# Performance work log

Hardware: AMD Instinct MI355X
Metric: run time of the kernel (lower is better)

The kernel has to match this reference:

```python
import math
import jax, jax.numpy as jnp
import numpy as np

N_NODES = 10000
N_EDGES = 160000
F_IN = 256
HID = 500
N_OUT = 100


def setup_inputs() -> dict:
    key = jax.random.key(0)
    ks = jax.random.split(key, 20)
    inp = {}
    inp['x'] = jax.random.normal(ks[0], (N_NODES, F_IN), jnp.float32)
    inp['edge_src'] = jax.random.randint(ks[1], (N_EDGES,), 0, N_NODES, jnp.int32)
    inp['edge_dst'] = jax.random.randint(ks[2], (N_EDGES,), 0, N_NODES, jnp.int32)
    inp['edge_weight'] = jax.random.uniform(ks[3], (N_EDGES,), jnp.float32)
    s1 = 1.0 / math.sqrt(F_IN)
    s2 = 1.0 / math.sqrt(HID)
    inp['W1_rel'] = jax.random.uniform(ks[4], (HID, F_IN), jnp.float32, -s1, s1)
    inp['b1'] = jax.random.uniform(ks[5], (HID,), jnp.float32, -s1, s1)
    inp['W1_root'] = jax.random.uniform(ks[6], (HID, F_IN), jnp.float32, -s1, s1)
    inp['p1_w'] = jax.random.uniform(ks[7], (HID,), jnp.float32, -s2, s2)
    inp['W2_rel'] = jax.random.uniform(ks[8], (HID, HID), jnp.float32, -s2, s2)
    inp['b2'] = jax.random.uniform(ks[9], (HID,), jnp.float32, -s2, s2)
    inp['W2_root'] = jax.random.uniform(ks[10], (HID, HID), jnp.float32, -s2, s2)
    inp['p2_w'] = jax.random.uniform(ks[11], (HID,), jnp.float32, -s2, s2)
    s3 = 1.0 / math.sqrt(1000)
    inp['lin1_W'] = jax.random.uniform(ks[12], (2000, 1000), jnp.float32, -s3, s3)
    inp['lin1_b'] = jax.random.uniform(ks[13], (2000,), jnp.float32, -s3, s3)
    s4 = 1.0 / math.sqrt(2000)
    inp['lin2_W'] = jax.random.uniform(ks[14], (4000, 2000), jnp.float32, -s4, s4)
    inp['lin2_b'] = jax.random.uniform(ks[15], (4000,), jnp.float32, -s4, s4)
    s5 = 1.0 / math.sqrt(4000)
    inp['lin3_W'] = jax.random.uniform(ks[16], (N_OUT, 4000), jnp.float32, -s5, s5)
    inp['lin3_b'] = jax.random.uniform(ks[17], (N_OUT,), jnp.float32, -s5, s5)
    return inp


def graph_conv(x, src, dst, w, W_rel, b_rel, W_root):
    # PyG GraphConv: out_i = W_rel @ sum_{j->i} w_ji * x_j + b + W_root @ x_i
    msg = x[src] * w[:, None]                              # [E, F]
    agg = jax.ops.segment_sum(msg, dst, num_segments=x.shape[0])
    return agg @ W_rel.T + b_rel + x @ W_root.T


def topk_pool(x, src, dst, w, p_w, ratio=0.5):
    # PyG TopKPooling: score = tanh(x @ p / ||p||); keep top-k; scale x by score.
    N = x.shape[0]
    k = int(math.ceil(ratio * N))
    score = jnp.tanh((x @ p_w) / jnp.linalg.norm(p_w))
    vals, perm = jax.lax.top_k(score, k)
    x_new = x[perm] * vals[:, None]
    # keep fixed-size edge list; dropped edges get weight 0 and point to node 0
    new_idx = jnp.zeros((N,), jnp.int32).at[perm].set(jnp.arange(k, dtype=jnp.int32))
    mask = jnp.zeros((N,), bool).at[perm].set(True)
    keep = mask[src] & mask[dst]
    src_new = jnp.where(keep, new_idx[src], 0)
    dst_new = jnp.where(keep, new_idx[dst], 0)
    w_new = jnp.where(keep, w, 0.0)
    return x_new, src_new, dst_new, w_new


def readout(x):
    # global max pool + global mean pool over the single graph -> [1, 2F]
    return jnp.concatenate([jnp.max(x, 0, keepdims=True), jnp.mean(x, 0, keepdims=True)], axis=1)


def reference(x, edge_src, edge_dst, edge_weight,
              W1_rel, b1, W1_root, p1_w,
              W2_rel, b2, W2_root, p2_w,
              lin1_W, lin1_b, lin2_W, lin2_b, lin3_W, lin3_b):
    h = jax.nn.relu(graph_conv(x, edge_src, edge_dst, edge_weight, W1_rel, b1, W1_root))
    h, s1, d1, w1 = topk_pool(h, edge_src, edge_dst, edge_weight, p1_w)
    x1 = readout(h)
    h = jax.nn.relu(graph_conv(h, s1, d1, w1, W2_rel, b2, W2_root))
    h, _, _, _ = topk_pool(h, s1, d1, w1, p2_w)
    x2 = readout(h)
    z = x1 + x2                                            # [1, 1000]
    z = jax.nn.relu(z @ lin1_W.T + lin1_b)
    z = jax.nn.relu(z @ lin2_W.T + lin2_b)                 # dropout is identity at eval
    return jax.nn.sigmoid(z @ lin3_W.T + lin3_b)
```

## Files before the change

kernel.cpp:

```cpp
#include <hip/hip_runtime.h>
#include <hip/hip_bf16.h>
#include <math.h>

#define NN1   10000
#define NE    160000
#define FIN   256
#define HID   500
#define K1    5000
#define NN2   5000
#define K2    2500

#define CSR_OFFS   0u
#define CSR_POS    10008u
#define CSR_SRC    20008u
#define CSR_W      180008u
#define OFF_AGG    340016u
#define OFF_H      2900016u
#define OFF_XP2    (OFF_H + 2500000u)
#define OFF_XP1    7900016u
#define OFF_SC1    10400016u
#define OFF_RK1    10410016u
#define OFF_SC2    10420016u
#define OFF_RK2    10425016u
#define OFF_RO     10430016u
#define OFF_Z      10432016u
#define OFF_T1     10433016u
#define OFF_T2     10435016u
#define OFF_INV    10439016u
#define OFF_CNT    10439024u
#define OFF_PM     10639024u
#define OFF_PS     10671024u
#define OFF_XB     10703024u
#define OFF_W1RB   11983024u
#define OFF_W1TB   12047024u
#define OFF_W2RB   12111024u
#define OFF_W2TB   12236024u
#define OFF_XP1B   12361024u
#define WS_FLOATS  13611024u

#define RCHUNK 500
#define ROSLAB1 64
#define ROSLAB2 32
#define RORPB   79

__device__ inline unsigned f2ord(float f) {
    unsigned u = __float_as_uint(f);
    return (u & 0x80000000u) ? ~u : (u | 0x80000000u);
}
__device__ inline unsigned long long rkey(float s, int j) {
    return ((unsigned long long)f2ord(s) << 32) | (unsigned)(0xFFFFFFFFu - (unsigned)j);
}
__device__ inline unsigned short bf16rn(float f) {
    unsigned u = __float_as_uint(f);
    u += 0x7FFFu + ((u >> 16) & 1u);
    return (unsigned short)(u >> 16);
}
__device__ inline float bf2f(unsigned short u) {
    return __uint_as_float((unsigned)u << 16);
}

typedef __attribute__((ext_vector_type(8))) short short8;
typedef __attribute__((ext_vector_type(4))) short short4v;
typedef __attribute__((ext_vector_type(4))) float floatx4;


__global__ __launch_bounds__(256) void k_prep(
    const float* __restrict__ x, unsigned short* __restrict__ xb,
    const float* __restrict__ w1r, unsigned short* __restrict__ w1rb,
    const float* __restrict__ w1t, unsigned short* __restrict__ w1tb,
    const float* __restrict__ w2r, unsigned short* __restrict__ w2rb,
    const float* __restrict__ w2t, unsigned short* __restrict__ w2tb,
    const float* __restrict__ p1, const float* __restrict__ p2,
    float* __restrict__ invn,
    const int* __restrict__ edst, int* __restrict__ pos) {
    __shared__ float red[256];
    int y = blockIdx.y;
    if (y < 5) {
        const float* s; unsigned short* d; int n;
        switch (y) {
            case 0: s = x;   d = xb;   n = NN1 * FIN; break;
            case 1: s = w1r; d = w1rb; n = HID * FIN; break;
            case 2: s = w1t; d = w1tb; n = HID * FIN; break;
            case 3: s = w2r; d = w2rb; n = HID * HID; break;
            default: s = w2t; d = w2tb; n = HID * HID; break;
        }
        int i = (blockIdx.x * 256 + threadIdx.x) * 4;
        if (i >= n) return;
        if (i + 3 < n) {
            float4 v = *(const float4*)(s + i);
            ushort4 o;
            o.x = bf16rn(v.x); o.y = bf16rn(v.y); o.z = bf16rn(v.z); o.w = bf16rn(v.w);
            *(ushort4*)(d + i) = o;
        } else {
            for (int q = 0; q < 4 && i + q < n; ++q) d[i + q] = bf16rn(s[i + q]);
        }
    } else if (y == 5) {
        if (blockIdx.x >= 2) return;
        const float* p = blockIdx.x ? p2 : p1;
        float s = 0.f;
        for (int i = threadIdx.x; i < HID; i += 256) { float v = p[i]; s += v * v; }
        red[threadIdx.x] = s; __syncthreads();
        for (int w = 128; w > 0; w >>= 1) {
            if (threadIdx.x < w) red[threadIdx.x] += red[threadIdx.x + w];
            __syncthreads();
        }
        if (threadIdx.x == 0) invn[blockIdx.x] = 1.0f / sqrtf(red[0]);
    } else {
        int e = blockIdx.x * 256 + threadIdx.x;
        if (e < NE) atomicAdd(&pos[edst[e]], 1);
    }
}

__global__ __launch_bounds__(1024) void k_scan(int* __restrict__ pos, int* __restrict__ offs) {
    __shared__ int tot[1024];
    int t = threadIdx.x;
    int base = t * 10;
    int loc[10]; int s = 0;
    #pragma unroll
    for (int q = 0; q < 10; ++q) {
        int v = (base + q < NN1) ? pos[base + q] : 0;
        loc[q] = s; s += v;
    }
    tot[t] = s; __syncthreads();
    for (int d = 1; d < 1024; d <<= 1) {
        int v = (t >= d) ? tot[t - d] : 0;
        __syncthreads();
        tot[t] += v;
        __syncthreads();
    }
    int excl = (t == 0) ? 0 : tot[t - 1];
    #pragma unroll
    for (int q = 0; q < 10; ++q)
        if (base + q < NN1) { int o = excl + loc[q]; offs[base + q] = o; pos[base + q] = o; }
    if (t == 1023) offs[NN1] = tot[1023];
}

__global__ void k_fill(const int* __restrict__ src, const int* __restrict__ dst,
                       const float* __restrict__ w, int* __restrict__ pos,
                       int* __restrict__ csrc, float* __restrict__ cw) {
    int e = blockIdx.x * 256 + threadIdx.x;
    if (e >= NE) return;
    int slot = atomicAdd(&pos[dst[e]], 1);
    csrc[slot] = src[e];
    cw[slot] = w[e];
}

__global__ __launch_bounds__(256) void k_gather1(
    const unsigned short* __restrict__ xb, const int* __restrict__ offs,
    const int* __restrict__ csrc, const float* __restrict__ cw,
    unsigned short* __restrict__ aggb) {
    int wave = (blockIdx.x * 256 + threadIdx.x) >> 6;
    int lane = threadIdx.x & 63;
    if (wave >= NN1) return;
    int b = offs[wave], e = offs[wave + 1];
    float4 acc = make_float4(0.f, 0.f, 0.f, 0.f);
    for (int p = b; p < e; ++p) {
        int s = csrc[p]; float we = cw[p];
        ushort4 u = *(const ushort4*)(xb + (size_t)s * FIN + lane * 4);
        acc.x += bf2f(u.x) * we; acc.y += bf2f(u.y) * we;
        acc.z += bf2f(u.z) * we; acc.w += bf2f(u.w) * we;
    }
    ushort4 o;
    o.x = bf16rn(acc.x); o.y = bf16rn(acc.y); o.z = bf16rn(acc.z); o.w = bf16rn(acc.w);
    *(ushort4*)(aggb + (size_t)wave * FIN + lane * 4) = o;
}

__global__ __launch_bounds__(256) void k_gather2(
    const unsigned short* __restrict__ Xb, const int* __restrict__ offs,
    const int* __restrict__ csrc, const float* __restrict__ cw,
    const int* __restrict__ rank, unsigned short* __restrict__ aggb) {
    int wave = (blockIdx.x * 256 + threadIdx.x) >> 6;
    int lane = threadIdx.x & 63;
    if (wave >= NN1) return;
    int rd = rank[wave];
    if (rd < 0) return;
    int b = offs[wave], e = offs[wave + 1];
    int c1 = 256 + lane * 4;
    float a0 = 0.f, a1 = 0.f, a2 = 0.f, a3 = 0.f;
    float b0 = 0.f, b1v = 0.f, b2 = 0.f, b3 = 0.f;
    for (int p = b; p < e; ++p) {
        int s = csrc[p];
        int rs = rank[s];
        if (rs < 0) continue;
        float we = cw[p];
        const unsigned short* row = Xb + (size_t)rs * HID;
        ushort4 u = *(const ushort4*)(row + lane * 4);
        a0 += bf2f(u.x) * we; a1 += bf2f(u.y) * we;
        a2 += bf2f(u.z) * we; a3 += bf2f(u.w) * we;
        if (c1 < HID) {
            ushort4 u2 = *(const ushort4*)(row + c1);
            b0 += bf2f(u2.x) * we; b1v += bf2f(u2.y) * we;
            b2 += bf2f(u2.z) * we; b3 += bf2f(u2.w) * we;
        }
    }
    unsigned short* o = aggb + (size_t)rd * HID;
    ushort4 o1; o1.x = bf16rn(a0); o1.y = bf16rn(a1); o1.z = bf16rn(a2); o1.w = bf16rn(a3);
    *(ushort4*)(o + lane * 4) = o1;
    if (c1 < HID) {
        ushort4 o2; o2.x = bf16rn(b0); o2.y = bf16rn(b1v); o2.z = bf16rn(b2); o2.w = bf16rn(b3);
        *(ushort4*)(o + c1) = o2;
    }
}

#define GBK 32
#define APAD 40
__global__ __launch_bounds__(256) void k_gemm_bf16(
    const unsigned short* __restrict__ A1, const unsigned short* __restrict__ B1,
    const unsigned short* __restrict__ A2, const unsigned short* __restrict__ B2,
    const float* __restrict__ bias, float* __restrict__ C,
    int M, int N, int Ka, int Kb, int nbyRow) {
    int b = blockIdx.x;
    int xcd = b & 7, seq = b >> 3;
    int colT = seq & 7;
    int rowT = xcd + 8 * (seq >> 3);
    if (rowT >= nbyRow) return;
    int row0 = rowT * 64, col0 = colT * 64;

    __shared__ unsigned short As[64 * APAD];
    __shared__ unsigned short Bs[64 * APAD];
    int tid = threadIdx.x;
    int lane = tid & 63, wid = tid >> 6;
    int waveM = wid & 1, waveN = wid >> 1;
    int quad = lane >> 4, mrow = lane & 15;
    floatx4 acc[2][2] = {};

    int sr = tid >> 2;
    int sk = (tid & 3) * 8;

    int nka = (Ka + GBK - 1) / GBK;
    int nkb = (Kb + GBK - 1) / GBK;
    int niter = nka + nkb;

    short4v pa0 = {0,0,0,0}, pa1 = {0,0,0,0}, pb0 = {0,0,0,0}, pb1 = {0,0,0,0};

    auto fetch = [&](const unsigned short* A, const unsigned short* B, int K, int k0) {
        int gr = row0 + sr, gn = col0 + sr, gk = k0 + sk;
        short4v z = {0,0,0,0};
        pa0 = z; pa1 = z; pb0 = z; pb1 = z;
        if (gr < M) {
            const unsigned short* p = A + (size_t)gr * K + gk;
            if (gk + 7 < K) { pa0 = *(const short4v*)p; pa1 = *(const short4v*)(p + 4); }
            else {
                unsigned short tmp[8] = {0,0,0,0,0,0,0,0};
                for (int q = 0; q < 8; ++q) if (gk + q < K) tmp[q] = p[q];
                pa0 = *(short4v*)&tmp[0]; pa1 = *(short4v*)&tmp[4];
            }
        }
        if (gn < N) {
            const unsigned short* p = B + (size_t)gn * K + gk;
            if (gk + 7 < K) { pb0 = *(const short4v*)p; pb1 = *(const short4v*)(p + 4); }
            else {
                unsigned short tmp[8] = {0,0,0,0,0,0,0,0};
                for (int q = 0; q < 8; ++q) if (gk + q < K) tmp[q] = p[q];
                pb0 = *(short4v*)&tmp[0]; pb1 = *(short4v*)&tmp[4];
            }
        }
    };

    fetch(A1, B1, Ka, 0);

    for (int it = 0; it < niter; ++it) {
        *(short4v*)&As[sr * APAD + sk]     = pa0;
        *(short4v*)&As[sr * APAD + sk + 4] = pa1;
        *(short4v*)&Bs[sr * APAD + sk]     = pb0;
        *(short4v*)&Bs[sr * APAD + sk + 4] = pb1;
        __syncthreads();
        if (it + 1 < niter) {
            int t = it + 1;
            int ph = (t >= nka);
            fetch(ph ? A2 : A1, ph ? B2 : B1, ph ? Kb : Ka, (ph ? t - nka : t) * GBK);
        }
        short8 bfr[2];
        #pragma unroll
        for (int nt = 0; nt < 2; ++nt)
            bfr[nt] = *(short8*)&Bs[(waveN * 32 + nt * 16 + mrow) * APAD + quad * 8];
        #pragma unroll
        for (int mt = 0; mt < 2; ++mt) {
            short8 afr = *(short8*)&As[(waveM * 32 + mt * 16 + mrow) * APAD + quad * 8];
            #pragma unroll
            for (int nt = 0; nt < 2; ++nt)
                acc[mt][nt] = __builtin_amdgcn_mfma_f32_16x16x32_bf16(
                    afr, bfr[nt], acc[mt][nt], 0, 0, 0);
        }
        __syncthreads();
    }
    #pragma unroll
    for (int nt = 0; nt < 2; ++nt) {
        int col = col0 + waveN * 32 + nt * 16 + mrow;
        if (col >= N) continue;
        float bv = bias[col];
        #pragma unroll
        for (int mt = 0; mt < 2; ++mt) {
            int rbase = row0 + waveM * 32 + mt * 16 + quad * 4;
            #pragma unroll
            for (int r = 0; r < 4; ++r) {
                int row = rbase + r;
                if (row < M) C[(size_t)row * N + col] = fmaxf(acc[mt][nt][r] + bv, 0.f);
            }
        }
    }
}

__global__ __launch_bounds__(256) void k_scores(
    const float* __restrict__ H, const float* __restrict__ p,
    const float* __restrict__ invnorm, float* __restrict__ score, int Nn) {
    int wave = (blockIdx.x * 256 + threadIdx.x) >> 6;
    int lane = threadIdx.x & 63;
    if (wave >= Nn) return;
    const float* h = H + (size_t)wave * HID;
    float s = 0.f;
    for (int i = lane; i < HID; i += 64) s += h[i] * p[i];
    for (int off = 32; off > 0; off >>= 1) s += __shfl_down(s, off, 64);
    if (lane == 0) score[wave] = tanhf(s * invnorm[0]);
}

__global__ __launch_bounds__(256) void k_rank_partial(
    const float* __restrict__ score, int* __restrict__ cntp, int Nn) {
    __shared__ unsigned long long kj[RCHUNK];
    int j0 = blockIdx.y * RCHUNK;
    int jn = min(Nn - j0, RCHUNK);
    for (int t = threadIdx.x; t < jn; t += 256)
        kj[t] = rkey(score[j0 + t], j0 + t);
    __syncthreads();
    int i = blockIdx.x * 256 + threadIdx.x;
    if (i >= Nn) return;
    unsigned long long ki = rkey(score[i], i);
    int c = 0;
    #pragma unroll 4
    for (int q = 0; q < jn; ++q)
        c += (kj[q] > ki) ? 1 : 0;
    cntp[(size_t)blockIdx.y * Nn + i] = c;
}

__global__ __launch_bounds__(128) void k_gather_pool(
    const float* __restrict__ H, const float* __restrict__ score,
    const int* __restrict__ cntp, int Nn, int nchunk, int kk,
    int* __restrict__ rank_out, float* __restrict__ Xp,
    unsigned short* __restrict__ Xb) {
    __shared__ int rsh;
    int i = blockIdx.x;
    if (threadIdx.x == 0) {
        int c = 0;
        for (int q = 0; q < nchunk; ++q) c += cntp[(size_t)q * Nn + i];
        int r = (c < kk) ? c : -1;
        if (rank_out) rank_out[i] = r;
        rsh = r;
    }
    __syncthreads();
    int r = rsh;
    if (r < 0) return;
    float sc = score[i];
    int c = threadIdx.x;
    if (c < HID / 4) {
        float4 v = *(const float4*)(H + (size_t)i * HID + c * 4);
        v.x *= sc; v.y *= sc; v.z *= sc; v.w *= sc;
        *(float4*)(Xp + (size_t)r * HID + c * 4) = v;
        if (Xb) {
            ushort4 o;
            o.x = bf16rn(v.x); o.y = bf16rn(v.y); o.z = bf16rn(v.z); o.w = bf16rn(v.w);
            *(ushort4*)(Xb + (size_t)r * HID + c * 4) = o;
        }
    }
}

__global__ __launch_bounds__(256) void k_readout_slab(
    const float* __restrict__ X, int rows, int rpb,
    float* __restrict__ pmax, float* __restrict__ psum) {
    __shared__ float4 lmx[4][64];
    __shared__ float4 lsm[4][64];
    int lane = threadIdx.x & 63;
    int rgrp = threadIdx.x >> 6;
    int c4 = blockIdx.x * 64 + lane;
    int r0 = blockIdx.y * rpb;
    int r1 = min(rows, r0 + rpb);
    float4 mx = make_float4(-INFINITY, -INFINITY, -INFINITY, -INFINITY);
    float4 sm = make_float4(0.f, 0.f, 0.f, 0.f);
    if (c4 < HID / 4) {
        for (int r = r0 + rgrp; r < r1; r += 4) {
            float4 v = *(const float4*)(X + (size_t)r * HID + c4 * 4);
            mx.x = fmaxf(mx.x, v.x); mx.y = fmaxf(mx.y, v.y);
            mx.z = fmaxf(mx.z, v.z); mx.w = fmaxf(mx.w, v.w);
            sm.x += v.x; sm.y += v.y; sm.z += v.z; sm.w += v.w;
        }
    }
    lmx[rgrp][lane] = mx; lsm[rgrp][lane] = sm;
    __syncthreads();
    if (rgrp == 0 && c4 < HID / 4) {
        #pragma unroll
        for (int g = 1; g < 4; ++g) {
            float4 m2 = lmx[g][lane], s2 = lsm[g][lane];
            mx.x = fmaxf(mx.x, m2.x); mx.y = fmaxf(mx.y, m2.y);
            mx.z = fmaxf(mx.z, m2.z); mx.w = fmaxf(mx.w, m2.w);
            sm.x += s2.x; sm.y += s2.y; sm.z += s2.z; sm.w += s2.w;
        }
        *(float4*)(pmax + (size_t)blockIdx.y * HID + c4 * 4) = mx;
        *(float4*)(psum + (size_t)blockIdx.y * HID + c4 * 4) = sm;
    }
}

__global__ __launch_bounds__(64) void k_ro_final(
    const float* __restrict__ pmax, const float* __restrict__ psum, int nslab,
    float* __restrict__ fmax, float* __restrict__ fsum) {
    int j = blockIdx.x * 64 + threadIdx.x;
    if (j >= HID) return;
    float mx = -INFINITY, sm = 0.f;
    for (int s = 0; s < nslab; ++s) {
        mx = fmaxf(mx, pmax[(size_t)s * HID + j]);
        sm += psum[(size_t)s * HID + j];
    }
    fmax[j] = mx; fsum[j] = sm;
}

__global__ __launch_bounds__(64) void k_ro2_combine(
    const float* __restrict__ pmax, const float* __restrict__ psum, int nslab,
    const float* __restrict__ max1, const float* __restrict__ sum1,
    float* __restrict__ z) {
    int j = blockIdx.x * 64 + threadIdx.x;
    if (j >= HID) return;
    float mx = -INFINITY, sm = 0.f;
    for (int s = 0; s < nslab; ++s) {
        mx = fmaxf(mx, pmax[(size_t)s * HID + j]);
        sm += psum[(size_t)s * HID + j];
    }
    z[j] = max1[j] + mx;
    z[HID + j] = sum1[j] * (1.0f / (float)K1) + sm * (1.0f / (float)K2);
}

__global__ __launch_bounds__(256) void k_mv(
    const float* __restrict__ v, const float* __restrict__ W,
    const float* __restrict__ bias, float* __restrict__ y,
    int rowsN, int K, int act) {
    int wave = (blockIdx.x * 256 + threadIdx.x) >> 6;
    int lane = threadIdx.x & 63;
    if (wave >= rowsN) return;
    const float* wr = W + (size_t)wave * K;
    float s = 0.f;
    for (int c = lane * 4; c < K; c += 256) {
        float4 a = *(const float4*)(wr + c);
        float4 xv = *(const float4*)(v + c);
        s += a.x * xv.x + a.y * xv.y + a.z * xv.z + a.w * xv.w;
    }
    for (int off = 32; off > 0; off >>= 1) s += __shfl_down(s, off, 64);
    if (lane == 0) {
        float r = s + bias[wave];
        y[wave] = (act == 0) ? fmaxf(r, 0.f) : 1.f / (1.f + expf(-r));
    }
}

extern "C" void kernel_launch(void* const* d_in, const int* in_sizes, int n_in,
                              void* d_out, int out_size, void* d_ws, size_t ws_size,
                              hipStream_t stream) {
    const float* x      = (const float*)d_in[0];
    const int*   esrc   = (const int*)d_in[1];
    const int*   edst   = (const int*)d_in[2];
    const float* ew     = (const float*)d_in[3];
    const float* W1_rel = (const float*)d_in[4];
    const float* b1     = (const float*)d_in[5];
    const float* W1_root= (const float*)d_in[6];
    const float* p1     = (const float*)d_in[7];
    const float* W2_rel = (const float*)d_in[8];
    const float* b2     = (const float*)d_in[9];
    const float* W2_root= (const float*)d_in[10];
    const float* p2     = (const float*)d_in[11];
    const float* l1W    = (const float*)d_in[12];
    const float* l1b    = (const float*)d_in[13];
    const float* l2W    = (const float*)d_in[14];
    const float* l2b    = (const float*)d_in[15];
    const float* l3W    = (const float*)d_in[16];
    const float* l3b    = (const float*)d_in[17];
    float* out = (float*)d_out;
    float* ws  = (float*)d_ws;

    if (ws_size < (size_t)WS_FLOATS * sizeof(float)) return;

    int*            offs  = (int*)(ws + CSR_OFFS);
    int*            pos   = (int*)(ws + CSR_POS);
    int*            csrc  = (int*)(ws + CSR_SRC);
    float*          cw    = ws + CSR_W;
    unsigned short* aggb  = (unsigned short*)(ws + OFF_AGG);
    float*          h     = ws + OFF_H;
    float*          xp1   = ws + OFF_XP1;
    float*          xp2   = ws + OFF_XP2;
    float*          sc1   = ws + OFF_SC1;
    int*            rk1   = (int*)(ws + OFF_RK1);
    float*          sc2   = ws + OFF_SC2;
    float*          max1  = ws + OFF_RO;
    float*          sum1  = ws + OFF_RO + 500;
    float*          zbuf  = ws + OFF_Z;
    float*          t1    = ws + OFF_T1;
    float*          t2    = ws + OFF_T2;
    float*          invn  = ws + OFF_INV;
    int*            cntp  = (int*)(ws + OFF_CNT);
    float*          pmax  = ws + OFF_PM;
    float*          psum  = ws + OFF_PS;
    unsigned short* xb    = (unsigned short*)(ws + OFF_XB);
    unsigned short* w1rb  = (unsigned short*)(ws + OFF_W1RB);
    unsigned short* w1tb  = (unsigned short*)(ws + OFF_W1TB);
    unsigned short* w2rb  = (unsigned short*)(ws + OFF_W2RB);
    unsigned short* w2tb  = (unsigned short*)(ws + OFF_W2TB);
    unsigned short* xp1b  = (unsigned short*)(ws + OFF_XP1B);

    hipMemsetAsync(pos, 0, NN1 * sizeof(int), stream);
    k_prep<<<dim3(2500, 7), 256, 0, stream>>>(
        x, xb, W1_rel, w1rb, W1_root, w1tb, W2_rel, w2rb, W2_root, w2tb,
        p1, p2, invn, edst, pos);
    k_scan<<<1, 1024, 0, stream>>>(pos, offs);
    k_fill<<<(NE + 255) / 256, 256, 0, stream>>>(esrc, edst, ew, pos, csrc, cw);

    k_gather1<<<(NN1 * 64 + 255) / 256, 256, 0, stream>>>(xb, offs, csrc, cw, aggb);
    {
        int nby = (NN1 + 63) / 64;
        int nblk = 64 * ((nby + 7) / 8);
        k_gemm_bf16<<<nblk, 256, 0, stream>>>(
            aggb, w1rb, xb, w1tb, b1, h, NN1, HID, FIN, FIN, nby);
    }

    k_scores<<<(NN1 * 64 + 255) / 256, 256, 0, stream>>>(h, p1, invn + 0, sc1, NN1);
    k_rank_partial<<<dim3((NN1 + 255) / 256, NN1 / RCHUNK), 256, 0, stream>>>(sc1, cntp, NN1);
    k_gather_pool<<<NN1, 128, 0, stream>>>(h, sc1, cntp, NN1, NN1 / RCHUNK, K1, rk1, xp1, xp1b);
    k_readout_slab<<<dim3(2, ROSLAB1), 256, 0, stream>>>(xp1, K1, RORPB, pmax, psum);
    k_ro_final<<<(HID + 63) / 64, 64, 0, stream>>>(pmax, psum, ROSLAB1, max1, sum1);

    k_gather2<<<(NN1 * 64 + 255) / 256, 256, 0, stream>>>(xp1b, offs, csrc, cw, rk1, aggb);
    {
        int nby = (NN2 + 63) / 64;
        int nblk = 64 * ((nby + 7) / 8);
        k_gemm_bf16<<<nblk, 256, 0, stream>>>(
            aggb, w2rb, xp1b, w2tb, b2, h, NN2, HID, HID, HID, nby);
    }

    k_scores<<<(NN2 * 64 + 255) / 256, 256, 0, stream>>>(h, p2, invn + 1, sc2, NN2);
    k_rank_partial<<<dim3((NN2 + 255) / 256, NN2 / RCHUNK), 256, 0, stream>>>(sc2, cntp, NN2);
    k_gather_pool<<<NN2, 128, 0, stream>>>(h, sc2, cntp, NN2, NN2 / RCHUNK, K2,
                                           (int*)nullptr, xp2, (unsigned short*)nullptr);
    k_readout_slab<<<dim3(2, ROSLAB2), 256, 0, stream>>>(xp2, K2, RORPB, pmax, psum);
    k_ro2_combine<<<(HID + 63) / 64, 64, 0, stream>>>(pmax, psum, ROSLAB2, max1, sum1, zbuf);

    k_mv<<<(2000 * 64) / 256, 256, 0, stream>>>(zbuf, l1W, l1b, t1, 2000, 1000, 0);
    k_mv<<<(4000 * 64) / 256, 256, 0, stream>>>(t1, l2W, l2b, t2, 4000, 2000, 0);
    k_mv<<<(100 * 64) / 256, 256, 0, stream>>>(t2, l3W, l3b, out, 100, 4000, 1);
}
```

Baseline: 363.7 us.

## Store activations in bf16, pack CSR edges, widen GEMM K-tile, parallelize rank sum

GEMM output and the pooled features are now stored in bf16 rather than fp32, so the score, pool and readout kernels read half as many bytes. CSR src and weight are packed into one int2 array, and the gather loops prefetch the next edge. The GEMM K-tile grows from 32 to 64 so each sync covers twice the MFMA work. The rank-count summation in gather_pool is spread across threads instead of done by one thread. The cost is extra bf16 rounding of the hidden activations, which could change top-k selection near ties.

Result: faster. 341.4 us (-6.1%).

```diff
diff --git a/kernel.cpp b/kernel.cpp
--- a/kernel.cpp
+++ b/kernel.cpp
@@ -12,8 +12,7 @@
 
 #define CSR_OFFS   0u
 #define CSR_POS    10008u
-#define CSR_SRC    20008u
-#define CSR_W      180008u
+#define CSR_EDGE   20008u
 #define OFF_AGG    340016u
 #define OFF_H      2900016u
 #define OFF_XP2    (OFF_H + 2500000u)
@@ -21,7 +20,6 @@
 #define OFF_SC1    10400016u
 #define OFF_RK1    10410016u
 #define OFF_SC2    10420016u
-#define OFF_RK2    10425016u
 #define OFF_RO     10430016u
 #define OFF_Z      10432016u
 #define OFF_T1     10433016u
@@ -60,7 +58,6 @@
 }
 
 typedef __attribute__((ext_vector_type(8))) short short8;
-typedef __attribute__((ext_vector_type(4))) short short4v;
 typedef __attribute__((ext_vector_type(4))) float floatx4;
 
 
@@ -137,26 +134,27 @@
 
 __global__ void k_fill(const int* __restrict__ src, const int* __restrict__ dst,
                        const float* __restrict__ w, int* __restrict__ pos,
-                       int* __restrict__ csrc, float* __restrict__ cw) {
+                       int2* __restrict__ ce) {
     int e = blockIdx.x * 256 + threadIdx.x;
     if (e >= NE) return;
     int slot = atomicAdd(&pos[dst[e]], 1);
-    csrc[slot] = src[e];
-    cw[slot] = w[e];
+    ce[slot] = make_int2(src[e], __float_as_int(w[e]));
 }
 
 __global__ __launch_bounds__(256) void k_gather1(
     const unsigned short* __restrict__ xb, const int* __restrict__ offs,
-    const int* __restrict__ csrc, const float* __restrict__ cw,
-    unsigned short* __restrict__ aggb) {
+    const int2* __restrict__ ce, unsigned short* __restrict__ aggb) {
     int wave = (blockIdx.x * 256 + threadIdx.x) >> 6;
     int lane = threadIdx.x & 63;
     if (wave >= NN1) return;
     int b = offs[wave], e = offs[wave + 1];
     float4 acc = make_float4(0.f, 0.f, 0.f, 0.f);
+    int2 nxt = (b < e) ? ce[b] : make_int2(0, 0);
     for (int p = b; p < e; ++p) {
-        int s = csrc[p]; float we = cw[p];
-        ushort4 u = *(const ushort4*)(xb + (size_t)s * FIN + lane * 4);
+        int2 cur = nxt;
+        if (p + 1 < e) nxt = ce[p + 1];
+        float we = __int_as_float(cur.y);
+        ushort4 u = *(const ushort4*)(xb + (size_t)cur.x * FIN + lane * 4);
         acc.x += bf2f(u.x) * we; acc.y += bf2f(u.y) * we;
         acc.z += bf2f(u.z) * we; acc.w += bf2f(u.w) * we;
     }
@@ -167,8 +165,8 @@
 
 __global__ __launch_bounds__(256) void k_gather2(
     const unsigned short* __restrict__ Xb, const int* __restrict__ offs,
-    const int* __restrict__ csrc, const float* __restrict__ cw,
-    const int* __restrict__ rank, unsigned short* __restrict__ aggb) {
+    const int2* __restrict__ ce, const int* __restrict__ rank,
+    unsigned short* __restrict__ aggb) {
     int wave = (blockIdx.x * 256 + threadIdx.x) >> 6;
     int lane = threadIdx.x & 63;
     if (wave >= NN1) return;
@@ -178,11 +176,13 @@
     int c1 = 256 + lane * 4;
     float a0 = 0.f, a1 = 0.f, a2 = 0.f, a3 = 0.f;
     float b0 = 0.f, b1v = 0.f, b2 = 0.f, b3 = 0.f;
+    int2 nxt = (b < e) ? ce[b] : make_int2(0, 0);
     for (int p = b; p < e; ++p) {
-        int s = csrc[p];
-        int rs = rank[s];
+        int2 cur = nxt;
+        if (p + 1 < e) nxt = ce[p + 1];
+        int rs = rank[cur.x];
         if (rs < 0) continue;
-        float we = cw[p];
+        float we = __int_as_float(cur.y);
         const unsigned short* row = Xb + (size_t)rs * HID;
         ushort4 u = *(const ushort4*)(row + lane * 4);
         a0 += bf2f(u.x) * we; a1 += bf2f(u.y) * we;
@@ -202,12 +202,19 @@
     }
 }
 
-#define GBK 32
-#define APAD 40
+__device__ inline short8 ld8g(const unsigned short* p, int gk, int K) {
+    if (gk + 7 < K) return *(const short8*)p;
+    unsigned short tmp[8] = {0,0,0,0,0,0,0,0};
+    for (int q = 0; q < 8; ++q) if (gk + q < K) tmp[q] = p[q];
+    return *(short8*)tmp;
+}
+
+#define GBK 64
+#define APAD 72
 __global__ __launch_bounds__(256) void k_gemm_bf16(
     const unsigned short* __restrict__ A1, const unsigned short* __restrict__ B1,
     const unsigned short* __restrict__ A2, const unsigned short* __restrict__ B2,
-    const float* __restrict__ bias, float* __restrict__ C,
+    const float* __restrict__ bias, unsigned short* __restrict__ C,
     int M, int N, int Ka, int Kb, int nbyRow) {
     int b = blockIdx.x;
     int xcd = b & 7, seq = b >> 3;
@@ -225,62 +232,56 @@
     floatx4 acc[2][2] = {};
 
     int sr = tid >> 2;
-    int sk = (tid & 3) * 8;
+    int sk = (tid & 3) * 16;
 
     int nka = (Ka + GBK - 1) / GBK;
     int nkb = (Kb + GBK - 1) / GBK;
     int niter = nka + nkb;
 
-    short4v pa0 = {0,0,0,0}, pa1 = {0,0,0,0}, pb0 = {0,0,0,0}, pb1 = {0,0,0,0};
+    short8 z8 = {0,0,0,0,0,0,0,0};
+    short8 paA = z8, paB = z8, pbA = z8, pbB = z8;
 
     auto fetch = [&](const unsigned short* A, const unsigned short* B, int K, int k0) {
         int gr = row0 + sr, gn = col0 + sr, gk = k0 + sk;
-        short4v z = {0,0,0,0};
-        pa0 = z; pa1 = z; pb0 = z; pb1 = z;
+        paA = z8; paB = z8; pbA = z8; pbB = z8;
         if (gr < M) {
             const unsigned short* p = A + (size_t)gr * K + gk;
-            if (gk + 7 < K) { pa0 = *(const short4v*)p; pa1 = *(const short4v*)(p + 4); }
-            else {
-                unsigned short tmp[8] = {0,0,0,0,0,0,0,0};
-                for (int q = 0; q < 8; ++q) if (gk + q < K) tmp[q] = p[q];
-                pa0 = *(short4v*)&tmp[0]; pa1 = *(short4v*)&tmp[4];
-            }
+            paA = ld8g(p, gk, K); paB = ld8g(p + 8, gk + 8, K);
         }
         if (gn < N) {
             const unsigned short* p = B + (size_t)gn * K + gk;
-            if (gk + 7 < K) { pb0 = *(const short4v*)p; pb1 = *(const short4v*)(p + 4); }
-            else {
-                unsigned short tmp[8] = {0,0,0,0,0,0,0,0};
-                for (int q = 0; q < 8; ++q) if (gk + q < K) tmp[q] = p[q];
-                pb0 = *(short4v*)&tmp[0]; pb1 = *(short4v*)&tmp[4];
-            }
+            pbA = ld8g(p, gk, K); pbB = ld8g(p + 8, gk + 8, K);
         }
     };
 
     fetch(A1, B1, Ka, 0);
 
     for (int it = 0; it < niter; ++it) {
-        *(short4v*)&As[sr * APAD + sk]     = pa0;
-        *(short4v*)&As[sr * APAD + sk + 4] = pa1;
-        *(short4v*)&Bs[sr * APAD + sk]     = pb0;
-        *(short4v*)&Bs[sr * APAD + sk + 4] = pb1;
+        *(short8*)&As[sr * APAD + sk]     = paA;
+        *(short8*)&As[sr * APAD + sk + 8] = paB;
+        *(short8*)&Bs[sr * APAD + sk]     = pbA;
+        *(short8*)&Bs[sr * APAD + sk + 8] = pbB;
         __syncthreads();
         if (it + 1 < niter) {
             int t = it + 1;
             int ph = (t >= nka);
             fetch(ph ? A2 : A1, ph ? B2 : B1, ph ? Kb : Ka, (ph ? t - nka : t) * GBK);
         }
-        short8 bfr[2];
         #pragma unroll
-        for (int nt = 0; nt < 2; ++nt)
-            bfr[nt] = *(short8*)&Bs[(waveN * 32 + nt * 16 + mrow) * APAD + quad * 8];
-        #pragma unroll
-        for (int mt = 0; mt < 2; ++mt) {
-            short8 afr = *(short8*)&As[(waveM * 32 + mt * 16 + mrow) * APAD + quad * 8];
+        for (int half = 0; half < 2; ++half) {
+            int ko = half * 32 + quad * 8;
+            short8 bfr[2];
             #pragma unroll
             for (int nt = 0; nt < 2; ++nt)
-                acc[mt][nt] = __builtin_amdgcn_mfma_f32_16x16x32_bf16(
-                    afr, bfr[nt], acc[mt][nt], 0, 0, 0);
+                bfr[nt] = *(short8*)&Bs[(waveN * 32 + nt * 16 + mrow) * APAD + ko];
+            #pragma unroll
+            for (int mt = 0; mt < 2; ++mt) {
+                short8 afr = *(short8*)&As[(waveM * 32 + mt * 16 + mrow) * APAD + ko];
+                #pragma unroll
+                for (int nt = 0; nt < 2; ++nt)
+                    acc[mt][nt] = __builtin_amdgcn_mfma_f32_16x16x32_bf16(
+                        afr, bfr[nt], acc[mt][nt], 0, 0, 0);
+            }
         }
         __syncthreads();
     }
@@ -295,21 +296,21 @@
             #pragma unroll
             for (int r = 0; r < 4; ++r) {
                 int row = rbase + r;
-                if (row < M) C[(size_t)row * N + col] = fmaxf(acc[mt][nt][r] + bv, 0.f);
+                if (row < M) C[(size_t)row * N + col] = bf16rn(fmaxf(acc[mt][nt][r] + bv, 0.f));
             }
         }
     }
 }
 
 __global__ __launch_bounds__(256) void k_scores(
-    const float* __restrict__ H, const float* __restrict__ p,
+    const unsigned short* __restrict__ Hb, const float* __restrict__ p,
     const float* __restrict__ invnorm, float* __restrict__ score, int Nn) {
     int wave = (blockIdx.x * 256 + threadIdx.x) >> 6;
     int lane = threadIdx.x & 63;
     if (wave >= Nn) return;
-    const float* h = H + (size_t)wave * HID;
+    const unsigned short* h = Hb + (size_t)wave * HID;
     float s = 0.f;
-    for (int i = lane; i < HID; i += 64) s += h[i] * p[i];
+    for (int i = lane; i < HID; i += 64) s += bf2f(h[i]) * p[i];
     for (int off = 32; off > 0; off >>= 1) s += __shfl_down(s, off, 64);
     if (lane == 0) score[wave] = tanhf(s * invnorm[0]);
 }
@@ -333,16 +334,21 @@
 }
 
 __global__ __launch_bounds__(128) void k_gather_pool(
-    const float* __restrict__ H, const float* __restrict__ score,
+    const unsigned short* __restrict__ Hb, const float* __restrict__ score,
     const int* __restrict__ cntp, int Nn, int nchunk, int kk,
-    int* __restrict__ rank_out, float* __restrict__ Xp,
-    unsigned short* __restrict__ Xb) {
+    int* __restrict__ rank_out, unsigned short* __restrict__ Xb) {
+    __shared__ int csum[128];
     __shared__ int rsh;
     int i = blockIdx.x;
+    int c = 0;
+    for (int q = threadIdx.x; q < nchunk; q += 128) c += cntp[(size_t)q * Nn + i];
+    csum[threadIdx.x] = c;
+    __syncthreads();
     if (threadIdx.x == 0) {
-        int c = 0;
-        for (int q = 0; q < nchunk; ++q) c += cntp[(size_t)q * Nn + i];
-        int r = (c < kk) ? c : -1;
+        int t = 0;
+        int lim = (nchunk < 128) ? nchunk : 128;
+        for (int q = 0; q < lim; ++q) t += csum[q];
+        int r = (t < kk) ? t : -1;
         if (rank_out) rank_out[i] = r;
         rsh = r;
     }
@@ -350,21 +356,18 @@
     int r = rsh;
     if (r < 0) return;
     float sc = score[i];
-    int c = threadIdx.x;
-    if (c < HID / 4) {
-        float4 v = *(const float4*)(H + (size_t)i * HID + c * 4);
-        v.x *= sc; v.y *= sc; v.z *= sc; v.w *= sc;
-        *(float4*)(Xp + (size_t)r * HID + c * 4) = v;
-        if (Xb) {
-            ushort4 o;
-            o.x = bf16rn(v.x); o.y = bf16rn(v.y); o.z = bf16rn(v.z); o.w = bf16rn(v.w);
-            *(ushort4*)(Xb + (size_t)r * HID + c * 4) = o;
-        }
+    int cc = threadIdx.x;
+    if (cc < HID / 4) {
+        ushort4 u = *(const ushort4*)(Hb + (size_t)i * HID + cc * 4);
+        ushort4 o;
+        o.x = bf16rn(bf2f(u.x) * sc); o.y = bf16rn(bf2f(u.y) * sc);
+        o.z = bf16rn(bf2f(u.z) * sc); o.w = bf16rn(bf2f(u.w) * sc);
+        *(ushort4*)(Xb + (size_t)r * HID + cc * 4) = o;
     }
 }
 
 __global__ __launch_bounds__(256) void k_readout_slab(
-    const float* __restrict__ X, int rows, int rpb,
+    const unsigned short* __restrict__ X, int rows, int rpb,
     float* __restrict__ pmax, float* __restrict__ psum) {
     __shared__ float4 lmx[4][64];
     __shared__ float4 lsm[4][64];
@@ -377,10 +380,11 @@
     float4 sm = make_float4(0.f, 0.f, 0.f, 0.f);
     if (c4 < HID / 4) {
         for (int r = r0 + rgrp; r < r1; r += 4) {
-            float4 v = *(const float4*)(X + (size_t)r * HID + c4 * 4);
-            mx.x = fmaxf(mx.x, v.x); mx.y = fmaxf(mx.y, v.y);
-            mx.z = fmaxf(mx.z, v.z); mx.w = fmaxf(mx.w, v.w);
-            sm.x += v.x; sm.y += v.y; sm.z += v.z; sm.w += v.w;
+            ushort4 u = *(const ushort4*)(X + (size_t)r * HID + c4 * 4);
+            float vx = bf2f(u.x), vy = bf2f(u.y), vz = bf2f(u.z), vw = bf2f(u.w);
+            mx.x = fmaxf(mx.x, vx); mx.y = fmaxf(mx.y, vy);
+            mx.z = fmaxf(mx.z, vz); mx.w = fmaxf(mx.w, vw);
+            sm.x += vx; sm.y += vy; sm.z += vz; sm.w += vw;
         }
     }
     lmx[rgrp][lane] = mx; lsm[rgrp][lane] = sm;
@@ -475,12 +479,10 @@
 
     int*            offs  = (int*)(ws + CSR_OFFS);
     int*            pos   = (int*)(ws + CSR_POS);
-    int*            csrc  = (int*)(ws + CSR_SRC);
-    float*          cw    = ws + CSR_W;
+    int2*           ce    = (int2*)(ws + CSR_EDGE);
     unsigned short* aggb  = (unsigned short*)(ws + OFF_AGG);
-    float*          h     = ws + OFF_H;
-    float*          xp1   = ws + OFF_XP1;
-    float*          xp2   = ws + OFF_XP2;
+    unsigned short* hb    = (unsigned short*)(ws + OFF_H);
+    unsigned short* xp2b  = (unsigned short*)(ws + OFF_XP2);
     float*          sc1   = ws + OFF_SC1;
     int*            rk1   = (int*)(ws + OFF_RK1);
     float*          sc2   = ws + OFF_SC2;
@@ -505,35 +507,35 @@
         x, xb, W1_rel, w1rb, W1_root, w1tb, W2_rel, w2rb, W2_root, w2tb,
         p1, p2, invn, edst, pos);
     k_scan<<<1, 1024, 0, stream>>>(pos, offs);
-    k_fill<<<(NE + 255) / 256, 256, 0, stream>>>(esrc, edst, ew, pos, csrc, cw);
-
-    k_gather1<<<(NN1 * 64 + 255) / 256, 256, 0, stream>>>(xb, offs, csrc, cw, aggb);
+    k_fill<<<(NE + 255) / 256, 256, 0, stream>>>(esrc, edst, ew, pos, ce);
+
+    k_gather1<<<(NN1 * 64 + 255) / 256, 256, 0, stream>>>(xb, offs, ce, aggb);
     {
         int nby = (NN1 + 63) / 64;
         int nblk = 64 * ((nby + 7) / 8);
         k_gemm_bf16<<<nblk, 256, 0, stream>>>(
-            aggb, w1rb, xb, w1tb, b1, h, NN1, HID, FIN, FIN, nby);
-    }
-
-    k_scores<<<(NN1 * 64 + 255) / 256, 256, 0, stream>>>(h, p1, invn + 0, sc1, NN1);
+            aggb, w1rb, xb, w1tb, b1, hb, NN1, HID, FIN, FIN, nby);
+    }
+
+    k_scores<<<(NN1 * 64 + 255) / 256, 256, 0, stream>>>(hb, p1, invn + 0, sc1, NN1);
     k_rank_partial<<<dim3((NN1 + 255) / 256, NN1 / RCHUNK), 256, 0, stream>>>(sc1, cntp, NN1);
-    k_gather_pool<<<NN1, 128, 0, stream>>>(h, sc1, cntp, NN1, NN1 / RCHUNK, K1, rk1, xp1, xp1b);
-    k_readout_slab<<<dim3(2, ROSLAB1), 256, 0, stream>>>(xp1, K1, RORPB, pmax, psum);
+    k_gather_pool<<<NN1, 128, 0, stream>>>(hb, sc1, cntp, NN1, NN1 / RCHUNK, K1, rk1, xp1b);
+    k_readout_slab<<<dim3(2, ROSLAB1), 256, 0, stream>>>(xp1b, K1, RORPB, pmax, psum);
     k_ro_final<<<(HID + 63) / 64, 64, 0, stream>>>(pmax, psum, ROSLAB1, max1, sum1);
 
-    k_gather2<<<(NN1 * 64 + 255) / 256, 256, 0, stream>>>(xp1b, offs, csrc, cw, rk1, aggb);
+    k_gather2<<<(NN1 * 64 + 255) / 256, 256, 0, stream>>>(xp1b, offs, ce, rk1, aggb);
     {
         int nby = (NN2 + 63) / 64;
         int nblk = 64 * ((nby + 7) / 8);
         k_gemm_bf16<<<nblk, 256, 0, stream>>>(
-            aggb, w2rb, xp1b, w2tb, b2, h, NN2, HID, HID, HID, nby);
-    }
-
-    k_scores<<<(NN2 * 64 + 255) / 256, 256, 0, stream>>>(h, p2, invn + 1, sc2, NN2);
+            aggb, w2rb, xp1b, w2tb, b2, hb, NN2, HID, HID, HID, nby);
+    }
+
+    k_scores<<<(NN2 * 64 + 255) / 256, 256, 0, stream>>>(hb, p2, invn + 1, sc2, NN2);
     k_rank_partial<<<dim3((NN2 + 255) / 256, NN2 / RCHUNK), 256, 0, stream>>>(sc2, cntp, NN2);
-    k_gather_pool<<<NN2, 128, 0, stream>>>(h, sc2, cntp, NN2, NN2 / RCHUNK, K2,
-                                           (int*)nullptr, xp2, (unsigned short*)nullptr);
-    k_readout_slab<<<dim3(2, ROSLAB2), 256, 0, stream>>>(xp2, K2, RORPB, pmax, psum);
+    k_gather_pool<<<NN2, 128, 0, stream>>>(hb, sc2, cntp, NN2, NN2 / RCHUNK, K2,
+                                           (int*)nullptr, xp2b);
+    k_readout_slab<<<dim3(2, ROSLAB2), 256, 0, stream>>>(xp2b, K2, RORPB, pmax, psum);
     k_ro2_combine<<<(HID + 63) / 64, 64, 0, stream>>>(pmax, psum, ROSLAB2, max1, sum1, zbuf);
 
     k_mv<<<(2000 * 64) / 256, 256, 0, stream>>>(zbuf, l1W, l1b, t1, 2000, 1000, 0);
```
